# Kernel tuning notes

Measured on AMD Instinct MI355X. Metric: run time of the kernel, lower is better.

The kernel has to match this reference:

```python
import jax, jax.numpy as jnp
import numpy as np

D = 768
H = 12
HD = D // H
NQ = 100
KV = 257
SEQ = NQ + KV
BS = 32


def layer_norm(x, g, b):
    # torch LayerNorm computed in fp32 then cast back (LayerNorm subclass)
    xf = x.astype(jnp.float32)
    m = xf.mean(-1, keepdims=True)
    v = ((xf - m) ** 2).mean(-1, keepdims=True)
    return ((xf - m) / jnp.sqrt(v + 1e-5) * g + b).astype(x.dtype)


def setup_inputs() -> dict:
    key = jax.random.key(0)
    ks = jax.random.split(key, 8)
    s = 0.02
    return {
        "y": jax.random.normal(ks[0], (SEQ, BS, D), jnp.float32),
        "attn_mask": jax.random.bernoulli(ks[1], 0.3, (BS, NQ, KV)),
        "in_proj_w": jax.random.normal(ks[2], (3 * D, D), jnp.float32) * s,
        "in_proj_b": jnp.zeros((3 * D,), jnp.float32),
        "new_q_w": jax.random.normal(ks[3], (D, D), jnp.float32) * s,
        "new_q_b": jnp.zeros((D,), jnp.float32),
        "out_w": jax.random.normal(ks[4], (D, D), jnp.float32) * s,
        "out_b": jnp.zeros((D,), jnp.float32),
        "ln1_g": jnp.ones((D,), jnp.float32),
        "ln1_b": jnp.zeros((D,), jnp.float32),
        "ln2_g": jnp.ones((D,), jnp.float32),
        "ln2_b": jnp.zeros((D,), jnp.float32),
        "fc_w": jax.random.normal(ks[5], (4 * D, D), jnp.float32) * s,
        "fc_b": jnp.zeros((4 * D,), jnp.float32),
        "proj_w": jax.random.normal(ks[6], (D, 4 * D), jnp.float32) * s,
        "proj_b": jnp.zeros((D,), jnp.float32),
    }


def _attention(x, attn_mask, in_proj_w, in_proj_b, new_q_w, new_q_b, out_w, out_b):
    # x: [seq, bs, D] (already ln_1'd); attn_mask: [bs, nq, kv] bool
    seq, bs, d = x.shape
    nq = attn_mask.shape[1]
    scale = 1.0 / np.sqrt(HD)
    # k/v (and the clip queries) come from the detached non-query tokens
    xkv = jax.lax.stop_gradient(x[nq:])  # [kv, bs, D]
    qkv = xkv @ in_proj_w.T + in_proj_b
    q, k, v = jnp.split(qkv, 3, axis=-1)

    def heads(t):  # [S, bs, D] -> [bs, H, S, hd]
        return t.reshape(t.shape[0], bs, H, HD).transpose(1, 2, 0, 3)

    q = heads(q) * scale
    k = heads(k)
    v = heads(v)
    # regular (clip) attention over shared k/v
    clip_attn = jnp.einsum('bhld,bhmd->bhlm', q, k)
    clip_out = jnp.einsum('bhlm,bhmd->bhld', jax.nn.softmax(clip_attn, axis=-1), v)
    # mask-conditioned queries via new_q_proj (NOT detached)
    new_q = heads(x[:nq] @ new_q_w.T + new_q_b) * scale  # [bs, H, nq, hd]
    bias = jnp.where(attn_mask[:, None], -jnp.inf, 0.0).astype(q.dtype)  # [bs,1,nq,kv]
    mask_attn = jnp.einsum('bhqd,bhmd->bhqm', new_q, k) + bias
    mask_out = jnp.einsum('bhqm,bhmd->bhqd', jax.nn.softmax(mask_attn, axis=-1), v)

    def merge(t):  # [bs, H, S, hd] -> [S, bs, D]
        return t.transpose(2, 0, 1, 3).reshape(t.shape[2], bs, d)

    attn_out = jnp.concatenate([merge(mask_out), merge(clip_out)], axis=0)
    return attn_out @ out_w.T + out_b


def reference(y, attn_mask, in_proj_w, in_proj_b, new_q_w, new_q_b, out_w, out_b,
              ln1_g, ln1_b, ln2_g, ln2_b, fc_w, fc_b, proj_w, proj_b):
    x = layer_norm(y, ln1_g, ln1_b)
    y = y + _attention(x, attn_mask, in_proj_w, in_proj_b, new_q_w, new_q_b, out_w, out_b)
    h = layer_norm(y, ln2_g, ln2_b)
    h = h @ fc_w.T + fc_b
    h = h * jax.nn.sigmoid(1.702 * h)  # QuickGELU
    return y + (h @ proj_w.T + proj_b)
```

## Files before the change

kernel.cpp:

```cpp
#include <hip/hip_runtime.h>


typedef short bf16x8 __attribute__((ext_vector_type(8)));
typedef float f32x4 __attribute__((ext_vector_type(4)));
typedef unsigned short u16;
typedef unsigned long long u64;

__device__ __forceinline__ u16 f2b(float f) {
    unsigned u = __builtin_bit_cast(unsigned, f);
    u = (u + 0x7fffu + ((u >> 16) & 1u)) >> 16;
    return (u16)u;
}
__device__ __forceinline__ float b2f(u16 h) {
    unsigned u = ((unsigned)h) << 16;
    return __builtin_bit_cast(float, u);
}
__device__ __forceinline__ unsigned pack2(float a, float b) {
    return (unsigned)f2b(a) | ((unsigned)f2b(b) << 16);
}
__device__ __forceinline__ void g2l16(const void* g, void* l) {
    __builtin_amdgcn_global_load_lds(
        (__attribute__((address_space(1))) void*)g,
        (__attribute__((address_space(3))) void*)l, 16, 0, 0);
}
#define MFMA16(a, b, c) __builtin_amdgcn_mfma_f32_16x16x32_bf16((a), (b), (c), 0, 0, 0)

__global__ __launch_bounds__(256) void cvt5_kernel(
    const float* __restrict__ s0, const float* __restrict__ s1, const float* __restrict__ s2,
    const float* __restrict__ s3, const float* __restrict__ s4, u16* __restrict__ dst)
{
    int i = blockIdx.x * 256 + threadIdx.x;
    int stride = gridDim.x * 256;
    for (; i < 1916928; i += stride) {
        const float* src; int off;
        if (i < 442368)       { src = s0; off = i; }
        else if (i < 589824)  { src = s1; off = i - 442368; }
        else if (i < 737280)  { src = s2; off = i - 589824; }
        else if (i < 1327104) { src = s3; off = i - 737280; }
        else                  { src = s4; off = i - 1327104; }
        float4 v = ((const float4*)src)[off];
        ushort4 o;
        o.x = f2b(v.x); o.y = f2b(v.y); o.z = f2b(v.z); o.w = f2b(v.w);
        ((ushort4*)dst)[i] = o;
    }
}

__global__ __launch_bounds__(256) void mask_pack(const int* __restrict__ m, u64* __restrict__ o) {
    int row = blockIdx.x * 4 + (threadIdx.x >> 6);
    int lane = threadIdx.x & 63;
    if (row >= 3200) return;
    const int* r = m + (size_t)row * 257;
    u64 w0 = __ballot(r[lane] != 0);
    u64 w1 = __ballot(r[64 + lane] != 0);
    u64 w2 = __ballot(r[128 + lane] != 0);
    u64 w3 = __ballot(r[192 + lane] != 0);
    u64 w4 = __ballot(lane == 0 && r[256] != 0);
    if (lane == 0) {
        u64* p = o + (size_t)row * 5;
        p[0] = w0; p[1] = w1; p[2] = w2; p[3] = w3; p[4] = w4;
    }
}

__global__ __launch_bounds__(256) void ln_kernel(
    const float* __restrict__ in, const float* __restrict__ g, const float* __restrict__ be,
    u16* __restrict__ out, int nrows)
{
    int row = blockIdx.x * 4 + (threadIdx.x >> 6);
    int lane = threadIdx.x & 63;
    if (row >= nrows) return;
    const float* p = in + (size_t)row * 768;
    float4 a0 = *(const float4*)(p + lane * 4);
    float4 a1 = *(const float4*)(p + 256 + lane * 4);
    float4 a2 = *(const float4*)(p + 512 + lane * 4);
    float s = a0.x + a0.y + a0.z + a0.w + a1.x + a1.y + a1.z + a1.w + a2.x + a2.y + a2.z + a2.w;
    for (int o = 32; o; o >>= 1) s += __shfl_xor(s, o);
    float mean = s * (1.f / 768.f);
    float vs = 0.f;
#define SQA(t) { float dx; dx = t.x-mean; vs += dx*dx; dx = t.y-mean; vs += dx*dx; dx = t.z-mean; vs += dx*dx; dx = t.w-mean; vs += dx*dx; }
    SQA(a0) SQA(a1) SQA(a2)
#undef SQA
    for (int o = 32; o; o >>= 1) vs += __shfl_xor(vs, o);
    float rstd = rsqrtf(vs * (1.f / 768.f) + 1e-5f);
    u16* orow = out + (size_t)row * 768;
#pragma unroll
    for (int i = 0; i < 3; ++i) {
        int d = i * 256 + lane * 4;
        float4 av = (i == 0) ? a0 : ((i == 1) ? a1 : a2);
        float4 gv = *(const float4*)(g + d);
        float4 bv = *(const float4*)(be + d);
        ushort4 ov;
        ov.x = f2b((av.x - mean) * rstd * gv.x + bv.x);
        ov.y = f2b((av.y - mean) * rstd * gv.y + bv.y);
        ov.z = f2b((av.z - mean) * rstd * gv.z + bv.z);
        ov.w = f2b((av.w - mean) * rstd * gv.w + bv.w);
        *(ushort4*)(orow + d) = ov;
    }
}

template<int ACT, int OUTBF, int RES>
__global__ __launch_bounds__(256) void gemm_bt(
    const u16* __restrict__ A, const u16* __restrict__ B,
    const float* __restrict__ bias, const float* __restrict__ res,
    void* __restrict__ Cp, int M, int N, int K)
{
    __shared__ u16 Al[2][128 * 32];
    __shared__ u16 Bl[2][128 * 32];
    const int t = threadIdx.x;
    const int lane = t & 63, w = t >> 6;
    const int wr = w >> 1, wc = w & 1;
    const int fr = lane & 15, fg = lane >> 4;

    const int raw = blockIdx.x + gridDim.x * blockIdx.y;
    const int rows_per = gridDim.x >> 3;
    const int gy = gridDim.y;
    const int xcd = raw & 7, idx = raw >> 3;
    const int nt = idx % gy;
    const int mt = xcd * rows_per + idx / gy;
    const int m0 = mt * 128, n0 = nt * 128;
    if (m0 >= M) return;

    const int srow = lane >> 2;
    const int scol = (lane & 3) * 8;
    int ar0 = m0 + w * 32 + srow;      int ar1 = ar0 + 16;
    ar0 = ar0 < M ? ar0 : M - 1;       ar1 = ar1 < M ? ar1 : M - 1;
    int br0 = n0 + w * 32 + srow;      int br1 = br0 + 16;
    br0 = br0 < N ? br0 : N - 1;       br1 = br1 < N ? br1 : N - 1;
    const u16* a0p = A + (size_t)ar0 * K + scol;
    const u16* a1p = A + (size_t)ar1 * K + scol;
    const u16* b0p = B + (size_t)br0 * K + scol;
    const u16* b1p = B + (size_t)br1 * K + scol;
    const int lo0 = (w * 2 + 0) * 512, lo1 = (w * 2 + 1) * 512;

    const int nk = K >> 5;
    g2l16(a0p, &Al[0][lo0]);
    g2l16(a1p, &Al[0][lo1]);
    g2l16(b0p, &Bl[0][lo0]);
    g2l16(b1p, &Bl[0][lo1]);
    __syncthreads();

    f32x4 acc[4][4] = {};
#pragma unroll 2
    for (int ki = 0; ki < nk; ++ki) {
        const int cur = ki & 1;
        if (ki + 1 < nk) {
            const int k0 = (ki + 1) << 5;
            const int nxt = cur ^ 1;
            g2l16(a0p + k0, &Al[nxt][lo0]);
            g2l16(a1p + k0, &Al[nxt][lo1]);
            g2l16(b0p + k0, &Bl[nxt][lo0]);
            g2l16(b1p + k0, &Bl[nxt][lo1]);
        }
        bf16x8 af[4], bfr[4];
#pragma unroll
        for (int m = 0; m < 4; ++m) af[m] = *(const bf16x8*)&Al[cur][(wr * 64 + m * 16 + fr) * 32 + fg * 8];
#pragma unroll
        for (int n = 0; n < 4; ++n) bfr[n] = *(const bf16x8*)&Bl[cur][(wc * 64 + n * 16 + fr) * 32 + fg * 8];
#pragma unroll
        for (int m = 0; m < 4; ++m)
#pragma unroll
            for (int n = 0; n < 4; ++n)
                acc[m][n] = MFMA16(af[m], bfr[n], acc[m][n]);
        __syncthreads();
    }
#pragma unroll
    for (int m = 0; m < 4; ++m) {
#pragma unroll
        for (int n = 0; n < 4; ++n) {
            int col = n0 + wc * 64 + n * 16 + fr;
            float bv = bias[col];
#pragma unroll
            for (int r = 0; r < 4; ++r) {
                int row = m0 + wr * 64 + m * 16 + fg * 4 + r;
                if (row < M) {
                    float v = acc[m][n][r] + bv;
                    if (RES) v += res[(size_t)row * N + col];
                    if (ACT) v = v / (1.f + __expf(-1.702f * v));
                    if (OUTBF) ((u16*)Cp)[(size_t)row * N + col] = f2b(v);
                    else       ((float*)Cp)[(size_t)row * N + col] = v;
                }
            }
        }
    }
}

__global__ __launch_bounds__(256, 2) void attn_kernel(
    const u16* __restrict__ qkv,
    const u16* __restrict__ nq,
    const u64* __restrict__ mpk,
    u16* __restrict__ out)
{
    __shared__ u16 Kl[272 * 64];
    __shared__ u16 Vt[64 * 296];
    __shared__ u16 Pb[4][640];
    const int raw = blockIdx.x;
    const int bid = (raw & 7) * 48 + (raw >> 3);
    const int b = bid / 12, h = bid % 12;
    const int t = threadIdx.x, lane = t & 63, wv = t >> 6;
    const int fr = lane & 15, fg = lane >> 4;

    for (int i = t; i < 2048; i += 256) {
        int d = i >> 5, c = 257 + (i & 31);
        if (c < 288) Vt[d * 296 + c] = 0;
    }
    {
        const int r8 = t >> 3, c8 = (t & 7) * 8;
        const u16* kb = qkv + 768 + h * 64 + c8;
        const u16* vb = qkv + 1536 + h * 64 + c8;
#pragma unroll 1
        for (int p = 0; p < 9; ++p) {
            int m = r8 + p * 32;
            if (m <= 256) {
                size_t go = (size_t)(m * 32 + b) * 2304;
                bf16x8 kv = *(const bf16x8*)(kb + go);
                int byte = m * 128 + c8 * 2;
                *(bf16x8*)((char*)Kl + (byte ^ ((m & 7) << 4))) = kv;
                bf16x8 vv = *(const bf16x8*)(vb + go);
#pragma unroll
                for (int j = 0; j < 8; ++j)
                    Vt[(c8 + j) * 296 + m] = (u16)vv[j];
            }
        }
    }
    __syncthreads();

    const int swzK = (fr & 7) << 4;
    char* pb = (char*)&Pb[wv][0];
    const char* KlB = (const char*)Kl;
    const char* VtB = (const char*)Vt;

    auto fetch = [&](int ti, bf16x8& q0v, bf16x8& q1v, u64* mw, bool& im) {
        int q = ti * 16 + fr;
        int qc = q < 357 ? q : 356;
        im = qc < 100;
        const u16* qp = im ? (nq + (size_t)(qc * 32 + b) * 768 + h * 64)
                           : (qkv + (size_t)((qc - 100) * 32 + b) * 2304 + h * 64);
        q0v = *(const bf16x8*)(qp + fg * 8);
        q1v = *(const bf16x8*)(qp + 32 + fg * 8);
        if (im) {
            const u64* mp = mpk + (size_t)(b * 100 + qc) * 5;
            mw[0] = mp[0]; mw[1] = mp[1]; mw[2] = mp[2]; mw[3] = mp[3]; mw[4] = mp[4];
        } else {
            mw[0] = mw[1] = mw[2] = mw[3] = mw[4] = 0;
        }
    };

    bf16x8 qf0, qf1, qn0, qn1;
    u64 mwc[5], mwn[5];
    bool imc, imn;
    fetch(wv, qf0, qf1, mwc, imc);

#pragma unroll 1
    for (int ti = wv; ti < 23; ti += 4) {
        f32x4 sc[17];
#pragma unroll
        for (int kt = 0; kt < 17; ++kt) {
            int rb = (kt * 16 + fr) * 128;
            bf16x8 ka0 = *(const bf16x8*)(KlB + ((rb + fg * 16) ^ swzK));
            bf16x8 ka1 = *(const bf16x8*)(KlB + ((rb + 64 + fg * 16) ^ swzK));
            f32x4 a = {0.f, 0.f, 0.f, 0.f};
            a = MFMA16(ka0, qf0, a);
            a = MFMA16(ka1, qf1, a);
            sc[kt] = a;
        }
        if (ti + 4 < 23) fetch(ti + 4, qn0, qn1, mwn, imn);
        float mx = -INFINITY;
#pragma unroll
        for (int kt = 0; kt < 17; ++kt) {
            u64 mw = (kt >> 2) == 0 ? mwc[0] : (kt >> 2) == 1 ? mwc[1] : (kt >> 2) == 2 ? mwc[2]
                   : (kt >> 2) == 3 ? mwc[3] : mwc[4];
#pragma unroll
            for (int r = 0; r < 4; ++r) {
                int key = kt * 16 + fg * 4 + r;
                bool bad = (key > 256) || (imc && ((mw >> (key & 63)) & 1ull));
                float s = bad ? -INFINITY : sc[kt][r];
                sc[kt][r] = s;
                mx = fmaxf(mx, s);
            }
        }
        mx = fmaxf(mx, __shfl_xor(mx, 16));
        mx = fmaxf(mx, __shfl_xor(mx, 32));
        float l = 0.f;
        unsigned pk[17][2];
#pragma unroll
        for (int kt = 0; kt < 17; ++kt) {
            float p0 = __expf((sc[kt][0] - mx) * 0.125f);
            float p1 = __expf((sc[kt][1] - mx) * 0.125f);
            float p2 = __expf((sc[kt][2] - mx) * 0.125f);
            float p3 = __expf((sc[kt][3] - mx) * 0.125f);
            l += (p0 + p1) + (p2 + p3);
            pk[kt][0] = pack2(p0, p1);
            pk[kt][1] = pack2(p2, p3);
        }
        l += __shfl_xor(l, 16);
        l += __shfl_xor(l, 32);
        f32x4 oc[4] = {};
#pragma unroll
        for (int c = 0; c < 9; ++c) {
            uint2 w0; w0.x = pk[2 * c][0]; w0.y = pk[2 * c][1];
            *(uint2*)(pb + fr * 80 + fg * 8) = w0;
            uint2 w1;
            if (c < 8) { w1.x = pk[2 * c + 1][0]; w1.y = pk[2 * c + 1][1]; }
            else       { w1.x = 0; w1.y = 0; }
            *(uint2*)(pb + fr * 80 + 32 + fg * 8) = w1;
            bf16x8 pf = *(const bf16x8*)(pb + fr * 80 + fg * 16);
#pragma unroll
            for (int dt = 0; dt < 4; ++dt) {
                bf16x8 vf = *(const bf16x8*)(VtB + (dt * 16 + fr) * 592 + c * 64 + fg * 16);
                oc[dt] = MFMA16(vf, pf, oc[dt]);
            }
        }
        int q = ti * 16 + fr;
        if (q < 357) {
            float rl = 1.f / l;
            u16* op = out + (size_t)(q * 32 + b) * 768 + h * 64 + fg * 4;
#pragma unroll
            for (int dt = 0; dt < 4; ++dt) {
                ushort4 ov;
                ov.x = f2b(oc[dt][0] * rl); ov.y = f2b(oc[dt][1] * rl);
                ov.z = f2b(oc[dt][2] * rl); ov.w = f2b(oc[dt][3] * rl);
                *(ushort4*)(op + dt * 16) = ov;
            }
        }
        if (ti + 4 < 23) {
            qf0 = qn0; qf1 = qn1; imc = imn;
            mwc[0] = mwn[0]; mwc[1] = mwn[1]; mwc[2] = mwn[2]; mwc[3] = mwn[3]; mwc[4] = mwn[4];
        }
    }
}

extern "C" void kernel_launch(void* const* d_in, const int* in_sizes, int n_in,
                              void* d_out, int out_size, void* d_ws, size_t ws_size,
                              hipStream_t stream)
{
    const float* y   = (const float*)d_in[0];
    const int*   msk = (const int*)  d_in[1];
    const float* ipw = (const float*)d_in[2];
    const float* ipb = (const float*)d_in[3];
    const float* nqw = (const float*)d_in[4];
    const float* nqb = (const float*)d_in[5];
    const float* ow  = (const float*)d_in[6];
    const float* ob  = (const float*)d_in[7];
    const float* l1g = (const float*)d_in[8];
    const float* l1b = (const float*)d_in[9];
    const float* l2g = (const float*)d_in[10];
    const float* l2b = (const float*)d_in[11];
    const float* fcw = (const float*)d_in[12];
    const float* fcb = (const float*)d_in[13];
    const float* pjw = (const float*)d_in[14];
    const float* pjb = (const float*)d_in[15];

    char* ws = (char*)d_ws;
    u16* x_b   = (u16*)(ws + 0);
    u16* qkv_b = (u16*)(ws + 17547264);
    u16* nq_b  = (u16*)(ws + 55443456);
    u16* ao_b  = (u16*)(ws + 60358656);
    u16* h1_b  = (u16*)(ws + 0);
    u16* h_b   = (u16*)(ws + 77905920);
    u64* mpk_b = (u64*)(ws + 77905920);
    u16* w_ip  = (u16*)(ws + 95453184);
    float* out = (float*)d_out;

    cvt5_kernel<<<2048, 256, 0, stream>>>(ipw, nqw, ow, fcw, pjw, w_ip);
    mask_pack<<<800, 256, 0, stream>>>(msk, mpk_b);

    u16* w_nq  = w_ip + 1769472;
    u16* w_out = w_nq + 589824;
    u16* w_fc  = w_out + 589824;
    u16* w_pj  = w_fc + 2359296;

    ln_kernel<<<2856, 256, 0, stream>>>(y, l1g, l1b, x_b, 11424);
    gemm_bt<0, 1, 0><<<dim3(72, 18), 256, 0, stream>>>(x_b + (size_t)3200 * 768, w_ip, ipb, nullptr, qkv_b, 8224, 2304, 768);
    gemm_bt<0, 1, 0><<<dim3(32, 6), 256, 0, stream>>>(x_b, w_nq, nqb, nullptr, nq_b, 3200, 768, 768);
    attn_kernel<<<384, 256, 0, stream>>>(qkv_b, nq_b, mpk_b, ao_b);
    gemm_bt<0, 0, 1><<<dim3(96, 6), 256, 0, stream>>>(ao_b, w_out, ob, y, out, 11424, 768, 768);
    ln_kernel<<<2856, 256, 0, stream>>>(out, l2g, l2b, h_b, 11424);
    gemm_bt<1, 1, 0><<<dim3(96, 24), 256, 0, stream>>>(h_b, w_fc, fcb, nullptr, h1_b, 11424, 3072, 768);
    gemm_bt<0, 0, 1><<<dim3(96, 6), 256, 0, stream>>>(h1_b, w_pj, pjb, out, out, 11424, 768, 3072);
}
```

Measured before the change: 449.2 us.

## Add direct global-to-register GEMM path without LDS for FC layer

Adds a DIRECT template variant of the GEMM that loads MFMA operand fragments straight from global memory into registers, double-buffered across K steps, with no LDS staging and no barriers. Only the fc GEMM (QuickGELU, K=768) uses it. The aim is to remove LDS round trips and __syncthreads stalls. In exchange, each wave now reads its A and B fragments from global memory itself, which adds redundant global/L2 traffic and uses more registers.

```diff
diff --git a/kernel.cpp b/kernel.cpp
--- a/kernel.cpp
+++ b/kernel.cpp
@@ -97,14 +97,12 @@
     }
 }
 
-template<int ACT, int OUTBF, int RES>
+template<int ACT, int OUTBF, int RES, int DIRECT>
 __global__ __launch_bounds__(256) void gemm_bt(
     const u16* __restrict__ A, const u16* __restrict__ B,
     const float* __restrict__ bias, const float* __restrict__ res,
     void* __restrict__ Cp, int M, int N, int K)
 {
-    __shared__ u16 Al[2][128 * 32];
-    __shared__ u16 Bl[2][128 * 32];
     const int t = threadIdx.x;
     const int lane = t & 63, w = t >> 6;
     const int wr = w >> 1, wc = w & 1;
@@ -119,48 +117,89 @@
     const int m0 = mt * 128, n0 = nt * 128;
     if (m0 >= M) return;
 
-    const int srow = lane >> 2;
-    const int scol = (lane & 3) * 8;
-    int ar0 = m0 + w * 32 + srow;      int ar1 = ar0 + 16;
-    ar0 = ar0 < M ? ar0 : M - 1;       ar1 = ar1 < M ? ar1 : M - 1;
-    int br0 = n0 + w * 32 + srow;      int br1 = br0 + 16;
-    br0 = br0 < N ? br0 : N - 1;       br1 = br1 < N ? br1 : N - 1;
-    const u16* a0p = A + (size_t)ar0 * K + scol;
-    const u16* a1p = A + (size_t)ar1 * K + scol;
-    const u16* b0p = B + (size_t)br0 * K + scol;
-    const u16* b1p = B + (size_t)br1 * K + scol;
-    const int lo0 = (w * 2 + 0) * 512, lo1 = (w * 2 + 1) * 512;
-
     const int nk = K >> 5;
-    g2l16(a0p, &Al[0][lo0]);
-    g2l16(a1p, &Al[0][lo1]);
-    g2l16(b0p, &Bl[0][lo0]);
-    g2l16(b1p, &Bl[0][lo1]);
-    __syncthreads();
-
     f32x4 acc[4][4] = {};
+
+    if constexpr (DIRECT) {
+        const u16* ap[4];
+        const u16* bp[4];
+#pragma unroll
+        for (int m = 0; m < 4; ++m) {
+            int r = m0 + wr * 64 + m * 16 + fr;
+            r = r < M ? r : M - 1;
+            ap[m] = A + (size_t)r * K + fg * 8;
+        }
+#pragma unroll
+        for (int n = 0; n < 4; ++n) {
+            int r = n0 + wc * 64 + n * 16 + fr;
+            bp[n] = B + (size_t)r * K + fg * 8;
+        }
+        bf16x8 a0[4], b0[4], a1[4], b1[4];
+        auto loadset = [&](bf16x8* aa, bf16x8* bb, int k0) {
+#pragma unroll
+            for (int m = 0; m < 4; ++m) aa[m] = *(const bf16x8*)(ap[m] + k0);
+#pragma unroll
+            for (int n = 0; n < 4; ++n) bb[n] = *(const bf16x8*)(bp[n] + k0);
+        };
+        auto mfmaset = [&](const bf16x8* aa, const bf16x8* bb) {
+#pragma unroll
+            for (int m = 0; m < 4; ++m)
+#pragma unroll
+                for (int n = 0; n < 4; ++n)
+                    acc[m][n] = MFMA16(aa[m], bb[n], acc[m][n]);
+        };
+        loadset(a0, b0, 0);
+#pragma unroll 1
+        for (int ki = 0; ki < nk; ki += 2) {
+            if (ki + 1 < nk) loadset(a1, b1, (ki + 1) << 5);
+            mfmaset(a0, b0);
+            if (ki + 2 < nk) loadset(a0, b0, (ki + 2) << 5);
+            if (ki + 1 < nk) mfmaset(a1, b1);
+        }
+    } else {
+        __shared__ u16 Al[2][128 * 32];
+        __shared__ u16 Bl[2][128 * 32];
+        const int srow = lane >> 2;
+        const int scol = (lane & 3) * 8;
+        int ar0 = m0 + w * 32 + srow;      int ar1 = ar0 + 16;
+        ar0 = ar0 < M ? ar0 : M - 1;       ar1 = ar1 < M ? ar1 : M - 1;
+        int br0 = n0 + w * 32 + srow;      int br1 = br0 + 16;
+        br0 = br0 < N ? br0 : N - 1;       br1 = br1 < N ? br1 : N - 1;
+        const u16* a0p = A + (size_t)ar0 * K + scol;
+        const u16* a1p = A + (size_t)ar1 * K + scol;
+        const u16* b0p = B + (size_t)br0 * K + scol;
+        const u16* b1p = B + (size_t)br1 * K + scol;
+        const int lo0 = (w * 2 + 0) * 512, lo1 = (w * 2 + 1) * 512;
+
+        g2l16(a0p, &Al[0][lo0]);
+        g2l16(a1p, &Al[0][lo1]);
+        g2l16(b0p, &Bl[0][lo0]);
+        g2l16(b1p, &Bl[0][lo1]);
+        __syncthreads();
+
 #pragma unroll 2
-    for (int ki = 0; ki < nk; ++ki) {
-        const int cur = ki & 1;
-        if (ki + 1 < nk) {
-            const int k0 = (ki + 1) << 5;
-            const int nxt = cur ^ 1;
-            g2l16(a0p + k0, &Al[nxt][lo0]);
-            g2l16(a1p + k0, &Al[nxt][lo1]);
-            g2l16(b0p + k0, &Bl[nxt][lo0]);
-            g2l16(b1p + k0, &Bl[nxt][lo1]);
-        }
-        bf16x8 af[4], bfr[4];
-#pragma unroll
-        for (int m = 0; m < 4; ++m) af[m] = *(const bf16x8*)&Al[cur][(wr * 64 + m * 16 + fr) * 32 + fg * 8];
-#pragma unroll
-        for (int n = 0; n < 4; ++n) bfr[n] = *(const bf16x8*)&Bl[cur][(wc * 64 + n * 16 + fr) * 32 + fg * 8];
-#pragma unroll
-        for (int m = 0; m < 4; ++m)
-#pragma unroll
-            for (int n = 0; n < 4; ++n)
-                acc[m][n] = MFMA16(af[m], bfr[n], acc[m][n]);
-        __syncthreads();
+        for (int ki = 0; ki < nk; ++ki) {
+            const int cur = ki & 1;
+            if (ki + 1 < nk) {
+                const int k0 = (ki + 1) << 5;
+                const int nxt = cur ^ 1;
+                g2l16(a0p + k0, &Al[nxt][lo0]);
+                g2l16(a1p + k0, &Al[nxt][lo1]);
+                g2l16(b0p + k0, &Bl[nxt][lo0]);
+                g2l16(b1p + k0, &Bl[nxt][lo1]);
+            }
+            bf16x8 af[4], bfr[4];
+#pragma unroll
+            for (int m = 0; m < 4; ++m) af[m] = *(const bf16x8*)&Al[cur][(wr * 64 + m * 16 + fr) * 32 + fg * 8];
+#pragma unroll
+            for (int n = 0; n < 4; ++n) bfr[n] = *(const bf16x8*)&Bl[cur][(wc * 64 + n * 16 + fr) * 32 + fg * 8];
+#pragma unroll
+            for (int m = 0; m < 4; ++m)
+#pragma unroll
+                for (int n = 0; n < 4; ++n)
+                    acc[m][n] = MFMA16(af[m], bfr[n], acc[m][n]);
+            __syncthreads();
+        }
     }
 #pragma unroll
     for (int m = 0; m < 4; ++m) {
@@ -369,11 +408,11 @@
     u16* w_pj  = w_fc + 2359296;
 
     ln_kernel<<<2856, 256, 0, stream>>>(y, l1g, l1b, x_b, 11424);
-    gemm_bt<0, 1, 0><<<dim3(72, 18), 256, 0, stream>>>(x_b + (size_t)3200 * 768, w_ip, ipb, nullptr, qkv_b, 8224, 2304, 768);
-    gemm_bt<0, 1, 0><<<dim3(32, 6), 256, 0, stream>>>(x_b, w_nq, nqb, nullptr, nq_b, 3200, 768, 768);
+    gemm_bt<0, 1, 0, 0><<<dim3(72, 18), 256, 0, stream>>>(x_b + (size_t)3200 * 768, w_ip, ipb, nullptr, qkv_b, 8224, 2304, 768);
+    gemm_bt<0, 1, 0, 0><<<dim3(32, 6), 256, 0, stream>>>(x_b, w_nq, nqb, nullptr, nq_b, 3200, 768, 768);
     attn_kernel<<<384, 256, 0, stream>>>(qkv_b, nq_b, mpk_b, ao_b);
-    gemm_bt<0, 0, 1><<<dim3(96, 6), 256, 0, stream>>>(ao_b, w_out, ob, y, out, 11424, 768, 768);
+    gemm_bt<0, 0, 1, 0><<<dim3(96, 6), 256, 0, stream>>>(ao_b, w_out, ob, y, out, 11424, 768, 768);
     ln_kernel<<<2856, 256, 0, stream>>>(out, l2g, l2b, h_b, 11424);
-    gemm_bt<1, 1, 0><<<dim3(96, 24), 256, 0, stream>>>(h_b, w_fc, fcb, nullptr, h1_b, 11424, 3072, 768);
-    gemm_bt<0, 0, 1><<<dim3(96, 6), 256, 0, stream>>>(h1_b, w_pj, pjb, out, out, 11424, 768, 3072);
-}
+    gemm_bt<1, 1, 0, 1><<<dim3(96, 24), 256, 0, stream>>>(h_b, w_fc, fcb, nullptr, h1_b, 11424, 3072, 768);
+    gemm_bt<0, 0, 1, 0><<<dim3(96, 6), 256, 0, stream>>>(h1_b, w_pj, pjb, out, out, 11424, 768, 3072);
+}
```

Result: slower. 570.3 us (+27.0%).
